# Kernel optimization log

Measured on AMD Instinct MI355X. Metric: run time of the kernel, lower is better.

## Reference

```python
import jax, jax.numpy as jnp
import numpy as np

B, T, C = 4, 2048, 1024
H, D, CS = 16, 64, 16   # heads, head dim, titans chunk size
EPS = 1e-5


def setup_inputs():
    key = jax.random.key(0)
    ks = jax.random.split(key, 4)
    s = 0.02
    return {
        "x": jax.random.normal(ks[0], (B, T, C), jnp.float32),
        "W_attn": jax.random.normal(ks[1], (C, 3 * C), jnp.float32) * s,
        "b_attn": jnp.zeros((3 * C,), jnp.float32),
        "W_param": jax.random.normal(ks[2], (C, 3 * H), jnp.float32) * s,
        "b_param": jnp.zeros((3 * H,), jnp.float32),
        "W_proj": jax.random.normal(ks[3], (C, C), jnp.float32) * s,
        "b_proj": jnp.zeros((C,), jnp.float32),
        "w": jnp.ones((H, D), jnp.float32),
        "b": jnp.zeros((H, D), jnp.float32),
    }


def _ln(x, w, b):
    # per-head layernorm over last dim
    mu = x.mean(-1, keepdims=True)
    xc = x - mu
    rstd = jax.lax.rsqrt((xc * xc).mean(-1, keepdims=True) + EPS)
    return xc * rstd * w + b


def _ln_bwd(x, w, dy):
    # gradient of layernorm(x; w, b) w.r.t. x, given upstream dy
    mu = x.mean(-1, keepdims=True)
    xc = x - mu
    rstd = jax.lax.rsqrt((xc * xc).mean(-1, keepdims=True) + EPS)
    xhat = xc * rstd
    wdy = dy * w
    c1 = (xhat * wdy).mean(-1, keepdims=True)
    c2 = wdy.mean(-1, keepdims=True)
    return (wdy - xhat * c1 - c2) * rstd


def _chunk_titans_linear(q, k, v, w, b, theta, alpha, eta):
    # q,k,v: [B,H,T,D]; theta/alpha/eta: [B,H,T,1]; w,b: [H,D]
    NT = T // CS
    wr = w.reshape(1, H, 1, D)
    br = b.reshape(1, H, 1, D)

    def to_chunks(t):
        return t.reshape(B, H, NT, CS, t.shape[-1]).transpose(2, 0, 1, 3, 4)

    qc, kc, vc = to_chunks(q), to_chunks(k), to_chunks(v)
    tc, ac, ec = to_chunks(theta), to_chunks(alpha), to_chunks(eta)

    def chunk_step(carry, inp):
        S, m = carry  # memory state / momentum: [B,H,D,D]
        q_i, k_i, v_i, th_i, al_i, et_i = inp
        # gradients of ||LN(k S) - v||^2 w.r.t. S, taken at the chunk-start state
        kh = jnp.einsum('bhcd,bhde->bhce', k_i, S)
        d_recon = 2.0 * (_ln(kh, wr, br) - v_i)
        dkh = _ln_bwd(kh, wr, d_recon)
        grads = jnp.einsum('bhci,bhcj->bhcij', k_i, dkh)  # [B,H,CS,D,D]

        def tok_step(c2, t_inp):
            S_t, m_t = c2
            g, th, al, et = t_inp
            th = th[..., None]; al = al[..., None]; et = et[..., None]
            m_t = et * m_t - th * g          # momentum
            S_t = (1.0 - al) * S_t + m_t     # weight-decayed state update
            return (S_t, m_t), S_t

        (S, m), S_seq = jax.lax.scan(
            tok_step, (S, m),
            (grads.transpose(2, 0, 1, 3, 4),
             th_i.transpose(2, 0, 1, 3),
             al_i.transpose(2, 0, 1, 3),
             et_i.transpose(2, 0, 1, 3)))
        # read memory with the freshly updated per-token state
        o_i = jnp.einsum('bhcd,cbhde->bhce', q_i, S_seq)
        return (S, m), o_i

    S0 = jnp.zeros((B, H, D, D), q.dtype)
    m0 = jnp.zeros((B, H, D, D), q.dtype)
    _, o_chunks = jax.lax.scan(chunk_step, (S0, m0), (qc, kc, vc, tc, ac, ec))
    o = o_chunks.transpose(1, 2, 0, 3, 4).reshape(B, H, T, D)
    return _ln(o, wr, br)  # normalized memory readout


def reference(x, W_attn, b_attn, W_param, b_param, W_proj, b_proj, w, b):
    qkv = x @ W_attn + b_attn
    q, k, v = jnp.split(qkv, 3, axis=-1)

    def heads(t):
        return t.reshape(B, T, H, D).transpose(0, 2, 1, 3)

    q, k, v = heads(q), heads(k), heads(v)
    q = q / jnp.maximum(jnp.linalg.norm(q, axis=-1, keepdims=True), 1e-12)
    k = k / jnp.maximum(jnp.linalg.norm(k, axis=-1, keepdims=True), 1e-12)
    p = jax.nn.sigmoid((x @ W_param + b_param).reshape(B, T, H, 3).transpose(0, 2, 1, 3))
    theta, alpha, eta = p[..., 0:1], p[..., 1:2], p[..., 2:3]
    o = _chunk_titans_linear(q, k, v, w, b, theta, alpha, eta)
    o = o.transpose(0, 2, 1, 3).reshape(B, T, C)
    return o @ W_proj + b_proj
```

## Files before the change

### kernel.cpp

```cpp
#include <hip/hip_runtime.h>
#include <cstddef>
#include <cstdint>
#include <math.h>

#define BB   4
#define TT   2048
#define CCH  1024
#define HH   16
#define DD   64
#define CSZ  16
#define NTC  128
#define EPSF 1e-5f
#define WVS  8

typedef __attribute__((ext_vector_type(8))) short bf16x8;
typedef __attribute__((ext_vector_type(4))) float f32x4;
typedef __attribute__((ext_vector_type(2))) float f32x2;

__device__ __forceinline__ uint32_t pack_split(float f) {
  uint32_t b = __float_as_uint(f);
  uint32_t uh = (b + 0x7fffu + ((b >> 16) & 1u)) >> 16;
  float fh = __uint_as_float(uh << 16);
  float r = f - fh;
  return uh | (__float_as_uint(r) & 0xffff0000u);
}
__device__ __forceinline__ float unpack_f(uint32_t u) {
  return __uint_as_float(u << 16) + __uint_as_float(u & 0xffff0000u);
}

__device__ __forceinline__ float wave_sum(float x) {
  float v = x;
  v += __int_as_float(__builtin_amdgcn_update_dpp(0, __float_as_int(v), 0x111, 0xf, 0xf, true));
  v += __int_as_float(__builtin_amdgcn_update_dpp(0, __float_as_int(v), 0x112, 0xf, 0xf, true));
  v += __int_as_float(__builtin_amdgcn_update_dpp(0, __float_as_int(v), 0x114, 0xf, 0xf, true));
  v += __int_as_float(__builtin_amdgcn_update_dpp(0, __float_as_int(v), 0x118, 0xf, 0xf, true));
  v += __int_as_float(__builtin_amdgcn_update_dpp(0, __float_as_int(v), 0x142, 0xa, 0xf, true));
  v += __int_as_float(__builtin_amdgcn_update_dpp(0, __float_as_int(v), 0x143, 0xc, 0xf, true));
  return __int_as_float(__builtin_amdgcn_readlane(__float_as_int(v), 63));
}

__device__ __forceinline__ float sigmoidf_(float x) {
  return 1.f / (1.f + expf(-x));
}

__global__ __launch_bounds__(256) void split_transpose(
    const float* __restrict__ W, uint32_t* __restrict__ Wt, int K, int N) {
  __shared__ float t[32][33];
  const int n0 = blockIdx.x * 32, k0 = blockIdx.y * 32;
  const int tx = threadIdx.x & 31, ty = threadIdx.x >> 5;
#pragma unroll
  for (int i = 0; i < 4; i++)
    t[ty + i * 8][tx] = W[(size_t)(k0 + ty + i * 8) * N + n0 + tx];
  __syncthreads();
#pragma unroll
  for (int i = 0; i < 4; i++)
    Wt[(size_t)(n0 + ty + i * 8) * K + k0 + tx] = pack_split(t[tx][ty + i * 8]);
}

template<bool A_PACKED, bool C_PACKED>
__global__ __launch_bounds__(256) void gemm_split(
    const void* __restrict__ Av, int lda,
    const uint32_t* __restrict__ Bt,
    const float* __restrict__ bias,
    void* __restrict__ Cv, int M, int N, int K) {
  __shared__ unsigned short Ahi[128][40];
  __shared__ unsigned short Alo[128][40];
  __shared__ unsigned short Bhi[128][40];
  __shared__ unsigned short Blo[128][40];

  const int tid = threadIdx.x;
  const int row0 = blockIdx.y * 128;
  const int col0 = blockIdx.x * 128;
  const int wv = tid >> 6;
  const int l  = tid & 63;
  const int wr = wv >> 1, wc = wv & 1;
  const int lrow = l & 15;
  const int kgrp = (l >> 4) * 8;

  const int sr = tid >> 1;
  const int sk = (tid & 1) * 16;

  f32x4 acc[4][4];
#pragma unroll
  for (int i = 0; i < 4; i++)
#pragma unroll
    for (int j = 0; j < 4; j++) acc[i][j] = (f32x4){0.f, 0.f, 0.f, 0.f};

  for (int k0 = 0; k0 < K; k0 += 32) {
    {
      uint32_t hp[8], lp[8];
      if (A_PACKED) {
        const uint32_t* Ap = (const uint32_t*)Av + (size_t)(row0 + sr) * lda + k0 + sk;
        uint32_t u[16];
#pragma unroll
        for (int i = 0; i < 4; i++) *(uint4*)&u[i * 4] = *(const uint4*)(Ap + i * 4);
#pragma unroll
        for (int j = 0; j < 8; j++) {
          hp[j] = (u[2 * j] & 0xffffu) | (u[2 * j + 1] << 16);
          lp[j] = (u[2 * j] >> 16) | (u[2 * j + 1] & 0xffff0000u);
        }
      } else {
        const float* Ap = (const float*)Av + (size_t)(row0 + sr) * lda + k0 + sk;
        float f[16];
#pragma unroll
        for (int i = 0; i < 4; i++) *(float4*)&f[i * 4] = *(const float4*)(Ap + i * 4);
        uint32_t uh[16], ulr[16];
#pragma unroll
        for (int j = 0; j < 16; j++) {
          uint32_t b = __float_as_uint(f[j]);
          uint32_t h = (b + 0x7fffu + ((b >> 16) & 1u)) >> 16;
          uh[j] = h;
          ulr[j] = __float_as_uint(f[j] - __uint_as_float(h << 16));
        }
#pragma unroll
        for (int j = 0; j < 8; j++) {
          hp[j] = uh[2 * j] | (uh[2 * j + 1] << 16);
          lp[j] = (ulr[2 * j] >> 16) | (ulr[2 * j + 1] & 0xffff0000u);
        }
      }
      *(uint4*)&Ahi[sr][sk]     = *(uint4*)&hp[0];
      *(uint4*)&Ahi[sr][sk + 8] = *(uint4*)&hp[4];
      *(uint4*)&Alo[sr][sk]     = *(uint4*)&lp[0];
      *(uint4*)&Alo[sr][sk + 8] = *(uint4*)&lp[4];
    }
    {
      const uint32_t* Bp = Bt + (size_t)(col0 + sr) * K + k0 + sk;
      uint32_t u[16], hp[8], lp[8];
#pragma unroll
      for (int i = 0; i < 4; i++) *(uint4*)&u[i * 4] = *(const uint4*)(Bp + i * 4);
#pragma unroll
      for (int j = 0; j < 8; j++) {
        hp[j] = (u[2 * j] & 0xffffu) | (u[2 * j + 1] << 16);
        lp[j] = (u[2 * j] >> 16) | (u[2 * j + 1] & 0xffff0000u);
      }
      *(uint4*)&Bhi[sr][sk]     = *(uint4*)&hp[0];
      *(uint4*)&Bhi[sr][sk + 8] = *(uint4*)&hp[4];
      *(uint4*)&Blo[sr][sk]     = *(uint4*)&lp[0];
      *(uint4*)&Blo[sr][sk + 8] = *(uint4*)&lp[4];
    }
    __syncthreads();

    bf16x8 bh[4], bl[4];
#pragma unroll
    for (int j = 0; j < 4; j++) {
      bh[j] = *(const bf16x8*)&Bhi[wc * 64 + j * 16 + lrow][kgrp];
      bl[j] = *(const bf16x8*)&Blo[wc * 64 + j * 16 + lrow][kgrp];
    }
#pragma unroll
    for (int i = 0; i < 4; i++) {
      bf16x8 ah = *(const bf16x8*)&Ahi[wr * 64 + i * 16 + lrow][kgrp];
      bf16x8 al = *(const bf16x8*)&Alo[wr * 64 + i * 16 + lrow][kgrp];
#pragma unroll
      for (int j = 0; j < 4; j++) {
        acc[i][j] = __builtin_amdgcn_mfma_f32_16x16x32_bf16(ah, bh[j], acc[i][j], 0, 0, 0);
        acc[i][j] = __builtin_amdgcn_mfma_f32_16x16x32_bf16(ah, bl[j], acc[i][j], 0, 0, 0);
        acc[i][j] = __builtin_amdgcn_mfma_f32_16x16x32_bf16(al, bh[j], acc[i][j], 0, 0, 0);
      }
    }
    __syncthreads();
  }

  const int crow4 = (l >> 4) * 4;
#pragma unroll
  for (int i = 0; i < 4; i++) {
#pragma unroll
    for (int j = 0; j < 4; j++) {
      const int col = col0 + wc * 64 + j * 16 + lrow;
      const float bv = bias[col];
      const int rowb = row0 + wr * 64 + i * 16 + crow4;
#pragma unroll
      for (int r = 0; r < 4; r++) {
        float v = acc[i][j][r] + bv;
        size_t off = (size_t)(rowb + r) * N + col;
        if (C_PACKED) ((uint32_t*)Cv)[off] = pack_split(v);
        else          ((float*)Cv)[off] = v;
      }
    }
  }
}

__global__ __launch_bounds__(256) void gemm_f32(
    const float* __restrict__ A, int lda,
    const float* __restrict__ W,
    const float* __restrict__ bias,
    float* __restrict__ C, int M, int N, int K) {
  __shared__ float As[16][132];
  __shared__ float Bs[16][128];
  const int tid  = threadIdx.x;
  const int row0 = blockIdx.y * 128;
  const int col0 = blockIdx.x * 128;
  const int ty = tid >> 4;
  const int tx = tid & 15;
  const int a_r = tid >> 2;
  const int a_k = (tid & 3) << 2;
  const int b_r = tid >> 5;
  const int b_c = (tid & 31) << 2;

  float acc[8][8];
#pragma unroll
  for (int i = 0; i < 8; i++)
#pragma unroll
    for (int j = 0; j < 8; j++) acc[i][j] = 0.f;

  float4 areg[2], breg[2];
  const int gc = col0 + b_c;
#pragma unroll
  for (int i = 0; i < 2; i++)
    areg[i] = *(const float4*)(A + (size_t)(row0 + a_r + i * 64) * lda + a_k);
#pragma unroll
  for (int i = 0; i < 2; i++) {
    breg[i] = make_float4(0.f, 0.f, 0.f, 0.f);
    if (gc < N) breg[i] = *(const float4*)(W + (size_t)(b_r + i * 8) * N + gc);
  }

  for (int k0 = 0; k0 < K; k0 += 16) {
#pragma unroll
    for (int i = 0; i < 2; i++) {
      int r = a_r + i * 64;
      As[a_k + 0][r] = areg[i].x;
      As[a_k + 1][r] = areg[i].y;
      As[a_k + 2][r] = areg[i].z;
      As[a_k + 3][r] = areg[i].w;
    }
#pragma unroll
    for (int i = 0; i < 2; i++) *(float4*)(&Bs[b_r + i * 8][b_c]) = breg[i];
    __syncthreads();

    if (k0 + 16 < K) {
#pragma unroll
      for (int i = 0; i < 2; i++)
        areg[i] = *(const float4*)(A + (size_t)(row0 + a_r + i * 64) * lda + (k0 + 16 + a_k));
#pragma unroll
      for (int i = 0; i < 2; i++) {
        breg[i] = make_float4(0.f, 0.f, 0.f, 0.f);
        if (gc < N) breg[i] = *(const float4*)(W + (size_t)(k0 + 16 + b_r + i * 8) * N + gc);
      }
    }

#pragma unroll
    for (int kk = 0; kk < 16; kk++) {
      float af[8], bf[8];
      *(float4*)&af[0] = *(const float4*)&As[kk][ty * 8];
      *(float4*)&af[4] = *(const float4*)&As[kk][ty * 8 + 4];
      *(float4*)&bf[0] = *(const float4*)&Bs[kk][tx * 8];
      *(float4*)&bf[4] = *(const float4*)&Bs[kk][tx * 8 + 4];
#pragma unroll
      for (int i = 0; i < 8; i++)
#pragma unroll
        for (int j = 0; j < 8; j++) acc[i][j] += af[i] * bf[j];
    }
    __syncthreads();
  }
#pragma unroll
  for (int i = 0; i < 8; i++) {
    int r = row0 + ty * 8 + i;
#pragma unroll
    for (int j0 = 0; j0 < 8; j0 += 4) {
      int cc = col0 + tx * 8 + j0;
      if (cc < N) {
        float4 ov;
        ov.x = acc[i][j0 + 0] + bias[cc + 0];
        ov.y = acc[i][j0 + 1] + bias[cc + 1];
        ov.z = acc[i][j0 + 2] + bias[cc + 2];
        ov.w = acc[i][j0 + 3] + bias[cc + 3];
        *(float4*)(C + (size_t)r * N + cc) = ov;
      }
    }
  }
}

__global__ __launch_bounds__(256) void normalize_qk(uint32_t* __restrict__ qkv) {
  const int idx = blockIdx.x * 4 + (threadIdx.x >> 6);
  const int l = threadIdx.x & 63;
  const int rowBT = idx >> 5;
  const int rem = idx & 31;
  const int which = rem >> 4;
  const int h = rem & 15;
  const size_t addr = (size_t)rowBT * 3072 + (size_t)which * 1024 + h * 64 + l;
  float v = unpack_f(qkv[addr]);
  float ss = wave_sum(v * v);
  float sc = 1.f / fmaxf(sqrtf(ss), 1e-12f);
  qkv[addr] = pack_split(v * sc);
}

__global__ __launch_bounds__(512) void titans_rec(
    uint32_t* __restrict__ qkv, const float* __restrict__ p,
    const float* __restrict__ w, const float* __restrict__ bparm) {
  const int bh = blockIdx.x;
  const int b = bh >> 4;
  const int h = bh & 15;
  const int tid = threadIdx.x;
  const int wv = tid >> 6;
  const int l = tid & 63;

  __shared__ float k_s[2][CSZ][DD];
  __shared__ float q_s[2][CSZ][DD];
  __shared__ float v_s[CSZ][DD];
  __shared__ float dkh_s[CSZ][DD];
  __shared__ float part[2][WVS][CSZ][DD];
  __shared__ float4 prm_s[2][CSZ];

  f32x2 S2[4], M2[4];
#pragma unroll
  for (int r = 0; r < 4; r++) { S2[r] = (f32x2){0.f, 0.f}; M2[r] = (f32x2){0.f, 0.f}; }

  const float w_l = w[h * DD + l];
  const float b_l = bparm[h * DD + l];

  uint32_t* qbase = qkv + (size_t)(b * TT) * 3072 + h * DD;
  const float* pbase = p + (size_t)(b * TT) * 48 + h * 3;

  uint32_t rq[2], rk[2], rv[2];
  float rp0 = 0.f, rp1 = 0.f, rp2 = 0.f;
  {
#pragma unroll
    for (int i = 0; i < 2; i++) {
      const int row = wv + i * 8;
      size_t roff = (size_t)row * 3072 + l;
      q_s[0][row][l] = unpack_f(qbase[roff]);
      k_s[0][row][l] = unpack_f(qbase[roff + 1024]);
      v_s[row][l]    = unpack_f(qbase[roff + 2048]);
    }
    if (tid < CSZ) {
      const float* pp = pbase + (size_t)tid * 48;
      prm_s[0][tid] = make_float4(sigmoidf_(pp[0]), sigmoidf_(pp[1]), sigmoidf_(pp[2]), 0.f);
    }
#pragma unroll
    for (int i = 0; i < 2; i++) {
      size_t roff = (size_t)(CSZ + wv + i * 8) * 3072 + l;
      rq[i] = qbase[roff];
      rk[i] = qbase[roff + 1024];
      rv[i] = qbase[roff + 2048];
    }
    if (tid < CSZ) {
      const float* pp = pbase + (size_t)(CSZ + tid) * 48;
      rp0 = pp[0]; rp1 = pp[1]; rp2 = pp[2];
    }
  }
  __syncthreads();

  for (int nt = 0; nt < NTC; nt++) {
    const int buf = nt & 1;
    float (*partw)[CSZ][DD] = part[buf];
    float (*partr)[CSZ][DD] = part[buf ^ 1];

    if (nt > 0) {
#pragma unroll
      for (int i = 0; i < 2; i++) {
        const int t = wv + i * 8;
        float o = 0.f;
#pragma unroll
        for (int ww = 0; ww < WVS; ww++) o += partr[ww][t][l];
        float mu = wave_sum(o) * (1.f / 64.f);
        float xc = o - mu;
        float var = wave_sum(xc * xc) * (1.f / 64.f);
        float rstd = rsqrtf(var + EPSF);
        float y = xc * rstd * w_l + b_l;
        qbase[(size_t)((nt - 1) * CSZ + t) * 3072 + 2048 + l] = pack_split(y);
      }
    }
#pragma unroll
    for (int c = 0; c < CSZ; c++) {
      const f32x2* kp2 = (const f32x2*)&k_s[buf][c][wv * 8];
      f32x2 a2;
      a2 = kp2[0] * S2[0];
      a2 = kp2[1] * S2[1] + a2;
      a2 = kp2[2] * S2[2] + a2;
      a2 = kp2[3] * S2[3] + a2;
      partw[wv][c][l] = a2.x + a2.y;
    }
    __syncthreads();

#pragma unroll
    for (int i = 0; i < 2; i++) {
      const int c = wv + i * 8;
      float kh = 0.f;
#pragma unroll
      for (int ww = 0; ww < WVS; ww++) kh += partw[ww][c][l];
      float mu = wave_sum(kh) * (1.f / 64.f);
      float xc = kh - mu;
      float var = wave_sum(xc * xc) * (1.f / 64.f);
      float rstd = rsqrtf(var + EPSF);
      float xhat = xc * rstd;
      float y = xhat * w_l + b_l;
      float dy = 2.f * (y - v_s[c][l]);
      float wdy = dy * w_l;
      float c1 = wave_sum(xhat * wdy) * (1.f / 64.f);
      float c2 = wave_sum(wdy) * (1.f / 64.f);
      dkh_s[c][l] = (wdy - xhat * c1 - c2) * rstd;
    }
    __syncthreads();

    if (nt + 1 < NTC) {
#pragma unroll
      for (int i = 0; i < 2; i++) {
        const int row = wv + i * 8;
        k_s[buf ^ 1][row][l] = unpack_f(rk[i]);
        q_s[buf ^ 1][row][l] = unpack_f(rq[i]);
        v_s[row][l] = unpack_f(rv[i]);
      }
      if (tid < CSZ)
        prm_s[buf ^ 1][tid] = make_float4(sigmoidf_(rp0), sigmoidf_(rp1), sigmoidf_(rp2), 0.f);
    }
    if (nt + 2 < NTC) {
#pragma unroll
      for (int i = 0; i < 2; i++) {
        size_t roff = (size_t)((nt + 2) * CSZ + wv + i * 8) * 3072 + l;
        rq[i] = qbase[roff];
        rk[i] = qbase[roff + 1024];
        rv[i] = qbase[roff + 2048];
      }
      if (tid < CSZ) {
        const float* pp = pbase + (size_t)((nt + 2) * CSZ + tid) * 48;
        rp0 = pp[0]; rp1 = pp[1]; rp2 = pp[2];
      }
    }
#pragma unroll
    for (int t = 0; t < CSZ; t++) {
      float4 prm = prm_s[buf][t];
      float a = prm.x * dkh_s[t][l];
      const f32x2 na2 = (f32x2){-a, -a};
      const f32x2 et2 = (f32x2){prm.z, prm.z};
      const f32x2 be2 = (f32x2){1.f - prm.y, 1.f - prm.y};
      const f32x2* kp2 = (const f32x2*)&k_s[buf][t][wv * 8];
      const f32x2* qp2 = (const f32x2*)&q_s[buf][t][wv * 8];
      f32x2 po2 = (f32x2){0.f, 0.f};
#pragma unroll
      for (int pq = 0; pq < 4; pq++) {
        M2[pq] = et2 * M2[pq] + na2 * kp2[pq];
        S2[pq] = be2 * S2[pq] + M2[pq];
        po2    = qp2[pq] * S2[pq] + po2;
      }
      partw[wv][t][l] = po2.x + po2.y;
    }
    __syncthreads();
  }

  {
    float (*partr)[CSZ][DD] = part[(NTC - 1) & 1];
#pragma unroll
    for (int i = 0; i < 2; i++) {
      const int t = wv + i * 8;
      float o = 0.f;
#pragma unroll
      for (int ww = 0; ww < WVS; ww++) o += partr[ww][t][l];
      float mu = wave_sum(o) * (1.f / 64.f);
      float xc = o - mu;
      float var = wave_sum(xc * xc) * (1.f / 64.f);
      float rstd = rsqrtf(var + EPSF);
      float y = xc * rstd * w_l + b_l;
      qbase[(size_t)((NTC - 1) * CSZ + t) * 3072 + 2048 + l] = pack_split(y);
    }
  }
}

extern "C" void kernel_launch(void* const* d_in, const int* in_sizes, int n_in,
                              void* d_out, int out_size, void* d_ws, size_t ws_size,
                              hipStream_t stream) {
  const float* x      = (const float*)d_in[0];
  const float* W_attn = (const float*)d_in[1];
  const float* b_attn = (const float*)d_in[2];
  const float* W_parm = (const float*)d_in[3];
  const float* b_parm = (const float*)d_in[4];
  const float* W_proj = (const float*)d_in[5];
  const float* b_proj = (const float*)d_in[6];
  const float* w      = (const float*)d_in[7];
  const float* bb     = (const float*)d_in[8];
  float* out = (float*)d_out;

  const int M = BB * TT;
  float* qkv = (float*)d_ws;
  float* pbf = qkv + (size_t)M * 3072;
  uint32_t* wattn_t = (uint32_t*)(pbf + (size_t)M * 48);
  uint32_t* wproj_t = wattn_t + (size_t)3072 * 1024;

  split_transpose<<<dim3(3072 / 32, 1024 / 32), 256, 0, stream>>>(W_attn, wattn_t, 1024, 3072);
  split_transpose<<<dim3(1024 / 32, 1024 / 32), 256, 0, stream>>>(W_proj, wproj_t, 1024, 1024);

  gemm_split<false, true><<<dim3(3072 / 128, M / 128), 256, 0, stream>>>(
      x, CCH, wattn_t, b_attn, qkv, M, 3072, CCH);
  gemm_f32<<<dim3(1, M / 128), 256, 0, stream>>>(x, CCH, W_parm, b_parm, pbf, M, 48, CCH);
  normalize_qk<<<(M * 2 * HH) / 4, 256, 0, stream>>>((uint32_t*)qkv);
  titans_rec<<<BB * HH, 512, 0, stream>>>((uint32_t*)qkv, pbf, w, bb);
  gemm_split<true, false><<<dim3(CCH / 128, M / 128), 256, 0, stream>>>(
      (uint32_t*)qkv + 2048, 3072, wproj_t, b_proj, out, M, CCH, CCH);
}
```

Baseline: 1.023 ms.

## Prefetch next GEMM tile into registers and use LDS-only barriers

The split-bf16 MFMA GEMM now loads the next K-tile from global memory into registers before the MFMA loop runs, so global latency overlaps with compute. Every __syncthreads is replaced by a barrier that waits only on LDS (lgkmcnt) and does not drain outstanding global loads (vmcnt). Without that change the register prefetch would stall at each barrier. The cost is more register pressure, which may lower occupancy. There is also a correctness risk if any barrier actually depended on global stores being visible.

```diff
diff --git a/kernel.cpp b/kernel.cpp
--- a/kernel.cpp
+++ b/kernel.cpp
@@ -16,6 +16,11 @@
 typedef __attribute__((ext_vector_type(8))) short bf16x8;
 typedef __attribute__((ext_vector_type(4))) float f32x4;
 typedef __attribute__((ext_vector_type(2))) float f32x2;
+
+__device__ __forceinline__ void bar_lds() {
+  asm volatile("s_waitcnt lgkmcnt(0)" ::: "memory");
+  __builtin_amdgcn_s_barrier();
+}
 
 __device__ __forceinline__ uint32_t pack_split(float f) {
   uint32_t b = __float_as_uint(f);
@@ -86,59 +91,79 @@
 #pragma unroll
     for (int j = 0; j < 4; j++) acc[i][j] = (f32x4){0.f, 0.f, 0.f, 0.f};
 
-  for (int k0 = 0; k0 < K; k0 += 32) {
-    {
-      uint32_t hp[8], lp[8];
-      if (A_PACKED) {
-        const uint32_t* Ap = (const uint32_t*)Av + (size_t)(row0 + sr) * lda + k0 + sk;
-        uint32_t u[16];
-#pragma unroll
-        for (int i = 0; i < 4; i++) *(uint4*)&u[i * 4] = *(const uint4*)(Ap + i * 4);
-#pragma unroll
-        for (int j = 0; j < 8; j++) {
-          hp[j] = (u[2 * j] & 0xffffu) | (u[2 * j + 1] << 16);
-          lp[j] = (u[2 * j] >> 16) | (u[2 * j + 1] & 0xffff0000u);
-        }
-      } else {
-        const float* Ap = (const float*)Av + (size_t)(row0 + sr) * lda + k0 + sk;
-        float f[16];
-#pragma unroll
-        for (int i = 0; i < 4; i++) *(float4*)&f[i * 4] = *(const float4*)(Ap + i * 4);
-        uint32_t uh[16], ulr[16];
-#pragma unroll
-        for (int j = 0; j < 16; j++) {
-          uint32_t b = __float_as_uint(f[j]);
-          uint32_t h = (b + 0x7fffu + ((b >> 16) & 1u)) >> 16;
-          uh[j] = h;
-          ulr[j] = __float_as_uint(f[j] - __uint_as_float(h << 16));
-        }
-#pragma unroll
-        for (int j = 0; j < 8; j++) {
-          hp[j] = uh[2 * j] | (uh[2 * j + 1] << 16);
-          lp[j] = (ulr[2 * j] >> 16) | (ulr[2 * j + 1] & 0xffff0000u);
-        }
-      }
-      *(uint4*)&Ahi[sr][sk]     = *(uint4*)&hp[0];
-      *(uint4*)&Ahi[sr][sk + 8] = *(uint4*)&hp[4];
-      *(uint4*)&Alo[sr][sk]     = *(uint4*)&lp[0];
-      *(uint4*)&Alo[sr][sk + 8] = *(uint4*)&lp[4];
-    }
-    {
-      const uint32_t* Bp = Bt + (size_t)(col0 + sr) * K + k0 + sk;
-      uint32_t u[16], hp[8], lp[8];
-#pragma unroll
-      for (int i = 0; i < 4; i++) *(uint4*)&u[i * 4] = *(const uint4*)(Bp + i * 4);
+  uint4 pa[4];
+  float4 pf[4];
+  uint4 pb[4];
+
+  auto load_tile = [&](int k0) {
+    if (A_PACKED) {
+      const uint32_t* Ap = (const uint32_t*)Av + (size_t)(row0 + sr) * lda + k0 + sk;
+#pragma unroll
+      for (int i = 0; i < 4; i++) pa[i] = *(const uint4*)(Ap + i * 4);
+    } else {
+      const float* Ap = (const float*)Av + (size_t)(row0 + sr) * lda + k0 + sk;
+#pragma unroll
+      for (int i = 0; i < 4; i++) pf[i] = *(const float4*)(Ap + i * 4);
+    }
+    const uint32_t* Bp = Bt + (size_t)(col0 + sr) * K + k0 + sk;
+#pragma unroll
+    for (int i = 0; i < 4; i++) pb[i] = *(const uint4*)(Bp + i * 4);
+  };
+
+  auto commit_tile = [&]() {
+    uint32_t hp[8], lp[8];
+    if (A_PACKED) {
+      uint32_t u[16];
+#pragma unroll
+      for (int i = 0; i < 4; i++) *(uint4*)&u[i * 4] = pa[i];
 #pragma unroll
       for (int j = 0; j < 8; j++) {
         hp[j] = (u[2 * j] & 0xffffu) | (u[2 * j + 1] << 16);
         lp[j] = (u[2 * j] >> 16) | (u[2 * j + 1] & 0xffff0000u);
       }
-      *(uint4*)&Bhi[sr][sk]     = *(uint4*)&hp[0];
-      *(uint4*)&Bhi[sr][sk + 8] = *(uint4*)&hp[4];
-      *(uint4*)&Blo[sr][sk]     = *(uint4*)&lp[0];
-      *(uint4*)&Blo[sr][sk + 8] = *(uint4*)&lp[4];
-    }
-    __syncthreads();
+    } else {
+      float f[16];
+#pragma unroll
+      for (int i = 0; i < 4; i++) *(float4*)&f[i * 4] = pf[i];
+      uint32_t uh[16], ulr[16];
+#pragma unroll
+      for (int j = 0; j < 16; j++) {
+        uint32_t b = __float_as_uint(f[j]);
+        uint32_t h = (b + 0x7fffu + ((b >> 16) & 1u)) >> 16;
+        uh[j] = h;
+        ulr[j] = __float_as_uint(f[j] - __uint_as_float(h << 16));
+      }
+#pragma unroll
+      for (int j = 0; j < 8; j++) {
+        hp[j] = uh[2 * j] | (uh[2 * j + 1] << 16);
+        lp[j] = (ulr[2 * j] >> 16) | (ulr[2 * j + 1] & 0xffff0000u);
+      }
+    }
+    *(uint4*)&Ahi[sr][sk]     = *(uint4*)&hp[0];
+    *(uint4*)&Ahi[sr][sk + 8] = *(uint4*)&hp[4];
+    *(uint4*)&Alo[sr][sk]     = *(uint4*)&lp[0];
+    *(uint4*)&Alo[sr][sk + 8] = *(uint4*)&lp[4];
+    {
+      uint32_t u[16], bh[8], bl[8];
+#pragma unroll
+      for (int i = 0; i < 4; i++) *(uint4*)&u[i * 4] = pb[i];
+#pragma unroll
+      for (int j = 0; j < 8; j++) {
+        bh[j] = (u[2 * j] & 0xffffu) | (u[2 * j + 1] << 16);
+        bl[j] = (u[2 * j] >> 16) | (u[2 * j + 1] & 0xffff0000u);
+      }
+      *(uint4*)&Bhi[sr][sk]     = *(uint4*)&bh[0];
+      *(uint4*)&Bhi[sr][sk + 8] = *(uint4*)&bh[4];
+      *(uint4*)&Blo[sr][sk]     = *(uint4*)&bl[0];
+      *(uint4*)&Blo[sr][sk + 8] = *(uint4*)&bl[4];
+    }
+  };
+
+  load_tile(0);
+  for (int k0 = 0; k0 < K; k0 += 32) {
+    commit_tile();
+    bar_lds();
+    if (k0 + 32 < K) load_tile(k0 + 32);
 
     bf16x8 bh[4], bl[4];
 #pragma unroll
@@ -157,7 +182,7 @@
         acc[i][j] = __builtin_amdgcn_mfma_f32_16x16x32_bf16(al, bh[j], acc[i][j], 0, 0, 0);
       }
     }
-    __syncthreads();
+    bar_lds();
   }
 
   const int crow4 = (l >> 4) * 4;
@@ -224,7 +249,7 @@
     }
 #pragma unroll
     for (int i = 0; i < 2; i++) *(float4*)(&Bs[b_r + i * 8][b_c]) = breg[i];
-    __syncthreads();
+    bar_lds();
 
     if (k0 + 16 < K) {
 #pragma unroll
@@ -249,7 +274,7 @@
 #pragma unroll
         for (int j = 0; j < 8; j++) acc[i][j] += af[i] * bf[j];
     }
-    __syncthreads();
+    bar_lds();
   }
 #pragma unroll
   for (int i = 0; i < 8; i++) {
@@ -337,7 +362,7 @@
       rp0 = pp[0]; rp1 = pp[1]; rp2 = pp[2];
     }
   }
-  __syncthreads();
+  bar_lds();
 
   for (int nt = 0; nt < NTC; nt++) {
     const int buf = nt & 1;
@@ -369,7 +394,7 @@
       a2 = kp2[3] * S2[3] + a2;
       partw[wv][c][l] = a2.x + a2.y;
     }
-    __syncthreads();
+    bar_lds();
 
 #pragma unroll
     for (int i = 0; i < 2; i++) {
@@ -389,7 +414,7 @@
       float c2 = wave_sum(wdy) * (1.f / 64.f);
       dkh_s[c][l] = (wdy - xhat * c1 - c2) * rstd;
     }
-    __syncthreads();
+    bar_lds();
 
     if (nt + 1 < NTC) {
 #pragma unroll
@@ -433,7 +458,7 @@
       }
       partw[wv][t][l] = po2.x + po2.y;
     }
-    __syncthreads();
+    bar_lds();
   }
 
   {
```

After: 977.4 us. -4.4%, faster.
